# Performance work log

Hardware: AMD Instinct MI355X
Metric: run time of the kernel (lower is better)

## Reference

```python
import jax, jax.numpy as jnp
import numpy as np

N_NODES = 50000
N_EDGES = 50000  # hyperedges
NNZ = 500000
N_GRAPHS = 50
IN_C, HID, OUT_C = 128, 256, 2


def _inv_deg(idx, num_segments):
    deg = jax.ops.segment_sum(jnp.ones(idx.shape[0], jnp.float32), idx, num_segments=num_segments)
    return jnp.where(deg > 0, 1.0 / deg, 0.0)


def hg_conv(x, W, b, rows, cols, dinv, binv):
    # PyG HypergraphConv (no attention, unit edge weights):
    # X' = D^{-1} H B^{-1} H^T (X Theta) + bias
    x = x @ W                                                    # [N, hid]
    e = jax.ops.segment_sum(x[rows], cols, num_segments=N_EDGES) * binv[:, None]   # edge feats [E, hid]
    out = jax.ops.segment_sum(e[cols], rows, num_segments=N_NODES) * dinv[:, None]  # node feats [N, hid]
    return out + b


def setup_inputs() -> dict:
    key = jax.random.key(0)
    ks = jax.random.split(key, 12)
    x = jax.random.normal(ks[0], (N_NODES, IN_C), jnp.float32)
    edge_index = jax.random.randint(ks[1], (2, NNZ), 0, N_EDGES, dtype=jnp.int64)
    batch = jnp.sort(jax.random.randint(ks[2], (N_NODES,), 0, N_GRAPHS, dtype=jnp.int64))
    s = 0.05
    return {
        "x": x, "edge_index": edge_index, "batch": batch,
        "W0": jax.random.normal(ks[3], (IN_C, HID), jnp.float32) * s,
        "b0": jnp.zeros((HID,), jnp.float32),
        "W1": jax.random.normal(ks[4], (HID, HID), jnp.float32) * s,
        "b1": jnp.zeros((HID,), jnp.float32),
        "W2": jax.random.normal(ks[5], (HID, HID), jnp.float32) * s,
        "b2": jnp.zeros((HID,), jnp.float32),
        "M1": jax.random.normal(ks[6], (HID, HID), jnp.float32) * s,
        "bM1": jnp.zeros((HID,), jnp.float32),
        "M2": jax.random.normal(ks[7], (HID, OUT_C), jnp.float32) * s,
        "bM2": jnp.zeros((OUT_C,), jnp.float32),
    }


def reference(x, edge_index, batch, W0, b0, W1, b1, W2, b2, M1, bM1, M2, bM2):
    rows, cols = edge_index[0], edge_index[1]
    dinv = _inv_deg(rows, N_NODES)   # node degree inverse
    binv = _inv_deg(cols, N_EDGES)   # hyperedge degree inverse
    h = jax.nn.relu(hg_conv(x, W0, b0, rows, cols, dinv, binv))
    h = jax.nn.relu(hg_conv(h, W1, b1, rows, cols, dinv, binv))
    h = jax.nn.relu(hg_conv(h, W2, b2, rows, cols, dinv, binv))
    # global_mean_pool (dropout is identity in eval mode)
    cnt = jax.ops.segment_sum(jnp.ones(N_NODES, jnp.float32), batch, num_segments=N_GRAPHS)
    pooled = jax.ops.segment_sum(h, batch, num_segments=N_GRAPHS) / jnp.maximum(cnt, 1.0)[:, None]
    # MLP head
    out = jax.nn.relu(pooled @ M1 + bM1) @ M2 + bM2
    return out
```

## Files before the change

kernel.cpp:

```cpp
#include <hip/hip_runtime.h>
#include <hip/hip_bf16.h>

#define NN   50000
#define NE   50000
#define NNZV 500000
#define NG   50
#define INC  128
#define HID  256
#define OUTC 2
#define STRIDE 32

typedef __bf16 bf16_t;
typedef __bf16 bf16x8 __attribute__((ext_vector_type(8)));
typedef float  f32x4  __attribute__((ext_vector_type(4)));
typedef float  f32x2  __attribute__((ext_vector_type(2)));

__device__ __forceinline__ bf16_t f2b(float f) {
  union { __hip_bfloat16 h; bf16_t b; } u;
  u.h = __float2bfloat16(f);
  return u.b;
}
__device__ __forceinline__ float b2f(bf16_t b) { return (float)b; }

template <bool HI>
__device__ __forceinline__ unsigned int fp8_pk2(float a, float b, unsigned int old) {
  return __builtin_amdgcn_cvt_pk_fp8_f32(a, b, old, HI);
}
__device__ __forceinline__ uint4 fp8_pk16(const float* v) {
  uint4 o;
  unsigned int* ow = &o.x;
#pragma unroll
  for (int wd = 0; wd < 4; wd++) {
    unsigned int u = fp8_pk2<false>(v[wd * 4 + 0], v[wd * 4 + 1], 0u);
    ow[wd] = fp8_pk2<true>(v[wd * 4 + 2], v[wd * 4 + 3], u);
  }
  return o;
}
__device__ __forceinline__ void fp8_acc16(uint4 v, f32x2* a2) {
  a2[0] += __builtin_amdgcn_cvt_pk_f32_fp8(v.x, false);
  a2[1] += __builtin_amdgcn_cvt_pk_f32_fp8(v.x, true);
  a2[2] += __builtin_amdgcn_cvt_pk_f32_fp8(v.y, false);
  a2[3] += __builtin_amdgcn_cvt_pk_f32_fp8(v.y, true);
  a2[4] += __builtin_amdgcn_cvt_pk_f32_fp8(v.z, false);
  a2[5] += __builtin_amdgcn_cvt_pk_f32_fp8(v.z, true);
  a2[6] += __builtin_amdgcn_cvt_pk_f32_fp8(v.w, false);
  a2[7] += __builtin_amdgcn_cvt_pk_f32_fp8(v.w, true);
}

__device__ __forceinline__ void wswiz_one(const float* __restrict__ W, bf16_t* __restrict__ wsw, int t) {
  int lane = t & 63;
  int nt   = (t >> 6) & 15;
  int kc   = t >> 10;
  int q = lane >> 4, n16 = lane & 15;
  bf16x8 o;
#pragma unroll
  for (int j = 0; j < 8; j++)
    o[j] = f2b(W[(size_t)(kc * 32 + q * 8 + j) * HID + nt * 16 + n16]);
  reinterpret_cast<bf16x8*>(wsw)[t] = o;
}

#define FILL_B ((NNZV + 255) / 256)
#define PREP_BX 1563
#define PREP_BW 80
#define PREP_BG 196

__global__ void build_kernel(const int* __restrict__ rows, const int* __restrict__ cols,
                             int* __restrict__ ncur, int* __restrict__ ecur,
                             unsigned short* __restrict__ ncol, unsigned short* __restrict__ erow,
                             const float* __restrict__ x, unsigned char* __restrict__ xb8,
                             const float* __restrict__ W0, const float* __restrict__ W1,
                             const float* __restrict__ W2, bf16_t* __restrict__ w0,
                             bf16_t* __restrict__ w1, bf16_t* __restrict__ w2,
                             const int* __restrict__ batch, int* __restrict__ gstart) {
  int blk = blockIdx.x;
  if (blk < FILL_B) {
    int i = blk * 256 + threadIdx.x;
    if (i < NNZV) {
      int r = rows[i], c = cols[i];
      int pe = atomicAdd(&ecur[c], 1);
      int pn = atomicAdd(&ncur[r], 1);
      if (pe < STRIDE) erow[((size_t)c << 5) + pe] = (unsigned short)r;
      if (pn < STRIDE) ncol[((size_t)r << 5) + pn] = (unsigned short)c;
    }
  } else if (blk < FILL_B + PREP_BX) {
    int t = (blk - FILL_B) * 256 + threadIdx.x;
    if (t >= NN * INC / 16) return;
    const f32x4* p = reinterpret_cast<const f32x4*>(x) + (size_t)t * 4;
    float v[16];
#pragma unroll
    for (int wd = 0; wd < 4; wd++) {
      f32x4 q4 = p[wd];
#pragma unroll
      for (int j = 0; j < 4; j++) v[wd * 4 + j] = q4[j];
    }
    reinterpret_cast<uint4*>(xb8)[t] = fp8_pk16(v);
  } else if (blk < FILL_B + PREP_BX + PREP_BW) {
    int t = (blk - FILL_B - PREP_BX) * 256 + threadIdx.x;
    const int C0 = (INC / 32) * 1024;
    const int C1 = (HID / 32) * 1024;
    if (t < C0)                wswiz_one(W0, w0, t);
    else if (t < C0 + C1)      wswiz_one(W1, w1, t - C0);
    else if (t < C0 + 2 * C1)  wswiz_one(W2, w2, t - C0 - C1);
  } else {
    int i = (blk - FILL_B - PREP_BX - PREP_BW) * 256 + threadIdx.x;
    if (i >= NN) return;
    int cur  = batch[i];
    int prev = (i == 0) ? -1 : batch[i - 1];
    for (int g = prev + 1; g <= cur; g++) gstart[g] = i;
    if (i == NN - 1) {
      for (int g = cur + 1; g <= NG; g++) gstart[g] = NN;
    }
  }
}

template <int K>
__device__ __forceinline__ void gather_direct(const unsigned char* __restrict__ src,
                                              const int* __restrict__ cnt,
                                              const unsigned short* __restrict__ lst,
                                              int seg, int lr, float* acc, int& c) {
  constexpr int LPR = K / 16;
  c = min(cnt[seg], STRIDE);
  const unsigned short* p = lst + ((size_t)seg << 5);
  const uint4* sv = reinterpret_cast<const uint4*>(src);
  f32x2* a2 = reinterpret_cast<f32x2*>(acc);
#pragma unroll
  for (int k = 0; k < 8; k++) a2[k] = f32x2{0.f, 0.f};
  for (int i0 = 0; i0 < c; i0 += 8) {
    int m = c - i0;
    uint4 v[8];
#pragma unroll
    for (int j = 0; j < 8; j++)
      if (j < m) v[j] = sv[(size_t)p[i0 + j] * LPR + lr];
#pragma unroll
    for (int j = 0; j < 8; j++)
      if (j < m) fp8_acc16(v[j], a2);
  }
}

template <int W>
__global__ __launch_bounds__(256) void seg_gather_kernel(const unsigned char* __restrict__ src,
                                                         const int* __restrict__ cnt,
                                                         const unsigned short* __restrict__ lst,
                                                         unsigned char* __restrict__ dst, int nseg) {
  constexpr int LPR = W / 16;
  constexpr int SPW = 64 / LPR;
  constexpr int SPB = 4 * SPW;
  const int lane = threadIdx.x & 63;
  const int wid  = threadIdx.x >> 6;
  const int sub  = lane / LPR, lr = lane % LPR;
  int seg = blockIdx.x * SPB + wid * SPW + sub;
  if (seg >= nseg) return;
  float acc[16];
  int c;
  gather_direct<W>(src, cnt, lst, seg, lr, acc, c);
  float sc = (c > 0) ? (1.0f / (float)c) : 0.f;
  float v16[16];
#pragma unroll
  for (int k = 0; k < 16; k++) v16[k] = acc[k] * sc;
  reinterpret_cast<uint4*>(dst + (size_t)seg * W + lr * 16)[0] = fp8_pk16(v16);
}

template <int K, bool GRELU, bool EPI, bool OUT8>
__global__ __launch_bounds__(256) void ngemm_kernel(const unsigned char* __restrict__ src,
                                                    const int* __restrict__ cnt,
                                                    const unsigned short* __restrict__ lst,
                                                    const float* __restrict__ gbias,
                                                    const bf16_t* __restrict__ wsw,
                                                    const float* __restrict__ ebias,
                                                    void* __restrict__ Bout, int M) {
  constexpr int SW = K + 8;
  __shared__ bf16_t arows[16 * SW];
  const int tid  = threadIdx.x;
  const int wid  = tid >> 6;
  const int lane = tid & 63;
  const int mblk = blockIdx.x * 16;

  constexpr int LPR = K / 16;
  constexpr int SPW = 64 / LPR;
  const int sub = lane / LPR, lr = lane % LPR;
  {
    int row = wid * SPW + sub;
    int seg = mblk + row;
    if (seg < M) {
      float acc[16];
      int c;
      gather_direct<K>(src, cnt, lst, seg, lr, acc, c);
      float sc = (c > 0) ? (1.0f / (float)c) : 0.f;
      bf16_t* dp = arows + row * SW + lr * 16;
      bf16x8 o0, o1;
#pragma unroll
      for (int k = 0; k < 8; k++) {
        float v0 = acc[k] * sc, v1 = acc[k + 8] * sc;
        if constexpr (GRELU) {
          v0 = fmaxf(v0 + gbias[lr * 16 + k], 0.f);
          v1 = fmaxf(v1 + gbias[lr * 16 + k + 8], 0.f);
        }
        o0[k] = f2b(v0);
        o1[k] = f2b(v1);
      }
      reinterpret_cast<bf16x8*>(dp)[0] = o0;
      reinterpret_cast<bf16x8*>(dp)[1] = o1;
    }
  }
  __syncthreads();

  const int q = lane >> 4, n16 = lane & 15;
  f32x4 acc2[4];
#pragma unroll
  for (int j = 0; j < 4; j++) acc2[j] = f32x4{0.f, 0.f, 0.f, 0.f};

  const bf16x8* wv = reinterpret_cast<const bf16x8*>(wsw);
  for (int kc = 0; kc < K / 32; kc++) {
    bf16x8 af = *reinterpret_cast<const bf16x8*>(arows + n16 * SW + kc * 32 + q * 8);
    const bf16x8* wp = wv + (size_t)kc * 1024 + (size_t)(wid * 4) * 64 + lane;
#pragma unroll
    for (int j = 0; j < 4; j++) {
      bf16x8 bf = wp[j * 64];
      acc2[j] = __builtin_amdgcn_mfma_f32_16x16x32_bf16(af, bf, acc2[j], 0, 0, 0);
    }
  }

  float bcol[4];
  if constexpr (EPI) {
#pragma unroll
    for (int j = 0; j < 4; j++) bcol[j] = ebias[(wid * 4 + j) * 16 + n16];
  }

  int mb = mblk + q * 4;
#pragma unroll
  for (int r = 0; r < 4; r++) {
    int m = mb + r;
    if (m < M) {
      if constexpr (OUT8) {
        unsigned char* dst = (unsigned char*)Bout + (size_t)m * HID + n16;
#pragma unroll
        for (int j = 0; j < 4; j++) {
          float v = acc2[j][r];
          if constexpr (EPI) v = fmaxf(v + bcol[j], 0.f);
          unsigned int wbits = fp8_pk2<false>(v, v, 0u);
          dst[(wid * 4 + j) << 4] = (unsigned char)(wbits & 0xffu);
        }
      } else {
        bf16_t* dst = (bf16_t*)Bout + (size_t)m * HID + n16;
#pragma unroll
        for (int j = 0; j < 4; j++) {
          float v = acc2[j][r];
          if constexpr (EPI) v = fmaxf(v + bcol[j], 0.f);
          dst[(wid * 4 + j) << 4] = f2b(v);
        }
      }
    }
  }
}

template <int K>
__global__ __launch_bounds__(256) void ngemm2_kernel(const unsigned char* __restrict__ src,
                                                     const int* __restrict__ cnt,
                                                     const unsigned short* __restrict__ lst,
                                                     const bf16_t* __restrict__ wswA,
                                                     const float* __restrict__ biasA,
                                                     const bf16_t* __restrict__ wswB,
                                                     unsigned char* __restrict__ Bout, int M) {
  constexpr int SW  = K + 8;
  constexpr int SW2 = HID + 8;
  constexpr int LPR = K / 16;
  constexpr int SPW = 64 / LPR;
  __shared__ bf16_t arows[32 * SW];
  __shared__ bf16_t brows[32 * SW2];
  const int tid  = threadIdx.x;
  const int wid  = tid >> 6;
  const int lane = tid & 63;
  const int mblk = blockIdx.x * 32;

  {
    const int sub = lane / LPR, lr = lane % LPR;
    int row = wid * SPW + sub;
    int seg = mblk + row;
    if (seg < M) {
      float acc[16];
      int c;
      gather_direct<K>(src, cnt, lst, seg, lr, acc, c);
      float sc = (c > 0) ? (1.0f / (float)c) : 0.f;
      bf16_t* dp = arows + row * SW + lr * 16;
      bf16x8 o0, o1;
#pragma unroll
      for (int k = 0; k < 8; k++) {
        o0[k] = f2b(acc[k] * sc);
        o1[k] = f2b(acc[k + 8] * sc);
      }
      reinterpret_cast<bf16x8*>(dp)[0] = o0;
      reinterpret_cast<bf16x8*>(dp)[1] = o1;
    }
  }
  __syncthreads();

  const int q = lane >> 4, n16 = lane & 15;
  {
    f32x4 acc2[2][4];
#pragma unroll
    for (int a = 0; a < 2; a++)
#pragma unroll
      for (int j = 0; j < 4; j++) acc2[a][j] = f32x4{0.f, 0.f, 0.f, 0.f};
    const bf16x8* wv = reinterpret_cast<const bf16x8*>(wswA);
    for (int kc = 0; kc < K / 32; kc++) {
      bf16x8 af0 = *reinterpret_cast<const bf16x8*>(arows + n16 * SW + kc * 32 + q * 8);
      bf16x8 af1 = *reinterpret_cast<const bf16x8*>(arows + (n16 + 16) * SW + kc * 32 + q * 8);
      const bf16x8* wp = wv + (size_t)kc * 1024 + (size_t)(wid * 4) * 64 + lane;
#pragma unroll
      for (int j = 0; j < 4; j++) {
        bf16x8 bf = wp[j * 64];
        acc2[0][j] = __builtin_amdgcn_mfma_f32_16x16x32_bf16(af0, bf, acc2[0][j], 0, 0, 0);
        acc2[1][j] = __builtin_amdgcn_mfma_f32_16x16x32_bf16(af1, bf, acc2[1][j], 0, 0, 0);
      }
    }
#pragma unroll
    for (int a = 0; a < 2; a++) {
#pragma unroll
      for (int j = 0; j < 4; j++) {
        float bj = biasA[(wid * 4 + j) * 16 + n16];
#pragma unroll
        for (int r = 0; r < 4; r++) {
          float v = fmaxf(acc2[a][j][r] + bj, 0.f);
          brows[(a * 16 + q * 4 + r) * SW2 + (wid * 4 + j) * 16 + n16] = f2b(v);
        }
      }
    }
  }
  __syncthreads();

  f32x4 acc3[2][4];
#pragma unroll
  for (int a = 0; a < 2; a++)
#pragma unroll
    for (int j = 0; j < 4; j++) acc3[a][j] = f32x4{0.f, 0.f, 0.f, 0.f};
  const bf16x8* wv = reinterpret_cast<const bf16x8*>(wswB);
  for (int kc = 0; kc < HID / 32; kc++) {
    bf16x8 af0 = *reinterpret_cast<const bf16x8*>(brows + n16 * SW2 + kc * 32 + q * 8);
    bf16x8 af1 = *reinterpret_cast<const bf16x8*>(brows + (n16 + 16) * SW2 + kc * 32 + q * 8);
    const bf16x8* wp = wv + (size_t)kc * 1024 + (size_t)(wid * 4) * 64 + lane;
#pragma unroll
    for (int j = 0; j < 4; j++) {
      bf16x8 bf = wp[j * 64];
      acc3[0][j] = __builtin_amdgcn_mfma_f32_16x16x32_bf16(af0, bf, acc3[0][j], 0, 0, 0);
      acc3[1][j] = __builtin_amdgcn_mfma_f32_16x16x32_bf16(af1, bf, acc3[1][j], 0, 0, 0);
    }
  }

#pragma unroll
  for (int a = 0; a < 2; a++) {
    int mb = mblk + a * 16 + q * 4;
#pragma unroll
    for (int r = 0; r < 4; r++) {
      int m = mb + r;
      if (m < M) {
        unsigned char* dst = Bout + (size_t)m * HID + n16;
#pragma unroll
        for (int j = 0; j < 4; j++) {
          float v = acc3[a][j][r];
          unsigned int wbits = fp8_pk2<false>(v, v, 0u);
          dst[(wid * 4 + j) << 4] = (unsigned char)(wbits & 0xffu);
        }
      }
    }
  }
}

__global__ __launch_bounds__(256) void npool_kernel(const unsigned char* __restrict__ src,
                                                    const int* __restrict__ cnt,
                                                    const unsigned short* __restrict__ lst,
                                                    const float* __restrict__ bias,
                                                    const int* __restrict__ batch,
                                                    float* __restrict__ pooled) {
  constexpr int K = HID, SW = K + 8;
  __shared__ bf16_t arows[16 * SW];
  const int tid  = threadIdx.x;
  const int wid  = tid >> 6;
  const int lane = tid & 63;
  const int mblk = blockIdx.x * 16;

  constexpr int LPR = K / 16;
  constexpr int SPW = 64 / LPR;
  const int sub = lane / LPR, lr = lane % LPR;
  {
    int row = wid * SPW + sub;
    int seg = mblk + row;
    if (seg < NN) {
      float acc[16];
      int c;
      gather_direct<K>(src, cnt, lst, seg, lr, acc, c);
      float sc = (c > 0) ? (1.0f / (float)c) : 0.f;
      bf16_t* dp = arows + row * SW + lr * 16;
      bf16x8 o0, o1;
#pragma unroll
      for (int k = 0; k < 8; k++) {
        o0[k] = f2b(fmaxf(acc[k] * sc + bias[lr * 16 + k], 0.f));
        o1[k] = f2b(fmaxf(acc[k + 8] * sc + bias[lr * 16 + k + 8], 0.f));
      }
      reinterpret_cast<bf16x8*>(dp)[0] = o0;
      reinterpret_cast<bf16x8*>(dp)[1] = o1;
    }
  }
  __syncthreads();

  int f = tid;
  float acc = 0.f;
  int curg = -1;
  for (int r = 0; r < 16; r++) {
    int node = mblk + r;
    if (node >= NN) break;
    int g = batch[node];
    if (g != curg) {
      if (curg >= 0) atomicAdd(&pooled[(size_t)curg * HID + f], acc);
      curg = g; acc = 0.f;
    }
    acc += b2f(arows[r * SW + f]);
  }
  if (curg >= 0) atomicAdd(&pooled[(size_t)curg * HID + f], acc);
}

__global__ void head_kernel(const float* __restrict__ pooled, const int* __restrict__ gstart,
                            const float* __restrict__ M1, const float* __restrict__ bM1,
                            const float* __restrict__ M2, const float* __restrict__ bM2,
                            float* __restrict__ out) {
  int g = blockIdx.x;
  int t = threadIdx.x;
  __shared__ float p[HID];
  __shared__ float red[256];
  float cntf = (float)(gstart[g + 1] - gstart[g]);
  float inv = 1.f / fmaxf(cntf, 1.f);
  p[t] = pooled[(size_t)g * HID + t] * inv;
  __syncthreads();
  float h = bM1[t];
  for (int k = 0; k < HID; k++) h += p[k] * M1[k * HID + t];
  h = fmaxf(h, 0.f);
  float c0 = h * M2[t * OUTC + 0];
  float c1 = h * M2[t * OUTC + 1];
  red[t] = c0;
  __syncthreads();
  for (int off = 128; off > 0; off >>= 1) {
    if (t < off) red[t] += red[t + off];
    __syncthreads();
  }
  float s0 = 0.f;
  if (t == 0) s0 = red[0];
  __syncthreads();
  red[t] = c1;
  __syncthreads();
  for (int off = 128; off > 0; off >>= 1) {
    if (t < off) red[t] += red[t + off];
    __syncthreads();
  }
  if (t == 0) {
    out[g * 2 + 0] = s0 + bM2[0];
    out[g * 2 + 1] = red[0] + bM2[1];
  }
}

extern "C" void kernel_launch(void* const* d_in, const int* in_sizes, int n_in,
                              void* d_out, int out_size, void* d_ws, size_t ws_size,
                              hipStream_t stream) {
  const float* x   = (const float*)d_in[0];
  const int* ei    = (const int*)d_in[1];
  const int* rows  = ei;
  const int* cols  = ei + NNZV;
  const int* batch = (const int*)d_in[2];
  const float* W0  = (const float*)d_in[3];
  const float* b0  = (const float*)d_in[4];
  const float* W1  = (const float*)d_in[5];
  const float* b1  = (const float*)d_in[6];
  const float* W2  = (const float*)d_in[7];
  const float* b2  = (const float*)d_in[8];
  const float* M1  = (const float*)d_in[9];
  const float* bM1 = (const float*)d_in[10];
  const float* M2  = (const float*)d_in[11];
  const float* bM2 = (const float*)d_in[12];
  float* out       = (float*)d_out;

  char* w = (char*)d_ws;
  size_t off = 0;
  bf16_t* P = (bf16_t*)(w + off); off += (size_t)NN * HID * 2;
  bf16_t* Q = (bf16_t*)(w + off); off += (size_t)NE * HID * 2;
  bf16_t* R = (bf16_t*)(w + off); off += (size_t)NN * HID * 2;
  bf16_t* wsw0 = (bf16_t*)(w + off); off += (size_t)INC * HID * 2;
  bf16_t* wsw1 = (bf16_t*)(w + off); off += (size_t)HID * HID * 2;
  bf16_t* wsw2 = (bf16_t*)(w + off); off += (size_t)HID * HID * 2;
  int* gstart   = (int*)(w + off);   off += (size_t)(NG + 1) * 4;
  size_t zoff = off;
  float* pooled = (float*)(w + off); off += (size_t)NG * HID * 4;
  int* ncur     = (int*)(w + off);   off += (size_t)NN * 4;
  int* ecur     = (int*)(w + off);   off += (size_t)NE * 4;
  size_t zbytes = off - zoff;
  off = (off + 63) & ~(size_t)63;
  unsigned short* erow = (unsigned short*)(w + off); off += (size_t)NE * STRIDE * 2;
  unsigned short* ncol = (unsigned short*)(w + off); off += (size_t)NN * STRIDE * 2;

  unsigned char* xb8 = (unsigned char*)R;
  unsigned char* Qe8 = (unsigned char*)Q;
  unsigned char* Q8  = (unsigned char*)Q;
  unsigned char* P8  = (unsigned char*)P;

  (void)hipMemsetAsync(w + zoff, 0, zbytes, stream);

  const int BN = 256;
  build_kernel<<<FILL_B + PREP_BX + PREP_BW + PREP_BG, BN, 0, stream>>>(
      rows, cols, ncur, ecur, ncol, erow, x, xb8, W0, W1, W2, wsw0, wsw1, wsw2, batch, gstart);

  seg_gather_kernel<INC><<<(NE + 31) / 32, BN, 0, stream>>>(xb8, ecur, erow, Qe8, NE);
  ngemm2_kernel<INC><<<(NN + 31) / 32, BN, 0, stream>>>(Qe8, ncur, ncol, wsw0, b0, wsw1, P8, NN);
  seg_gather_kernel<HID><<<(NE + 15) / 16, BN, 0, stream>>>(P8, ecur, erow, Q8, NE);
  ngemm_kernel<HID, true, false, true><<<(NN + 15) / 16, BN, 0, stream>>>(
      Q8, ncur, ncol, b1, wsw2, nullptr, P8, NN);
  seg_gather_kernel<HID><<<(NE + 15) / 16, BN, 0, stream>>>(P8, ecur, erow, Q8, NE);
  npool_kernel<<<(NN + 15) / 16, BN, 0, stream>>>(Q8, ncur, ncol, b2, batch, pooled);

  head_kernel<<<NG, 256, 0, stream>>>(pooled, gstart, M1, bM1, M2, bM2, out);
}
```

Before: 364.2 us.

## Partition CSR fill atomics by XCD using index low bits

Splits the adjacency-list build into separate edge-list and node-list passes, each replicated over 8 block groups that only handle indices whose low 3 bits match the block's position mod 8. This aims to keep atomic counter updates and list writes for a given index local to one XCD's L2 on a multi-die GPU, reducing cross-die atomic traffic. In exchange, every block rereads the rows/cols input 16 times and many more blocks are launched, with most threads doing no atomic work.

After: 332.5 us. -8.7%, faster.

```diff
diff --git a/kernel.cpp b/kernel.cpp
--- a/kernel.cpp
+++ b/kernel.cpp
@@ -59,7 +59,10 @@
   reinterpret_cast<bf16x8*>(wsw)[t] = o;
 }
 
-#define FILL_B ((NNZV + 255) / 256)
+#define FILL_EPT   2
+#define FILL_CHUNK (256 * FILL_EPT)
+#define FILL_NCH   ((NNZV + FILL_CHUNK - 1) / FILL_CHUNK)
+#define FILL_B     (FILL_NCH * 8)
 #define PREP_BX 1563
 #define PREP_BW 80
 #define PREP_BG 196
@@ -73,17 +76,32 @@
                              bf16_t* __restrict__ w1, bf16_t* __restrict__ w2,
                              const int* __restrict__ batch, int* __restrict__ gstart) {
   int blk = blockIdx.x;
-  if (blk < FILL_B) {
-    int i = blk * 256 + threadIdx.x;
-    if (i < NNZV) {
-      int r = rows[i], c = cols[i];
-      int pe = atomicAdd(&ecur[c], 1);
-      int pn = atomicAdd(&ncur[r], 1);
-      if (pe < STRIDE) erow[((size_t)c << 5) + pe] = (unsigned short)r;
-      if (pn < STRIDE) ncol[((size_t)r << 5) + pn] = (unsigned short)c;
-    }
-  } else if (blk < FILL_B + PREP_BX) {
-    int t = (blk - FILL_B) * 256 + threadIdx.x;
+  if (blk < 2 * FILL_B) {
+    bool ner = blk >= FILL_B;
+    int local = ner ? blk - FILL_B : blk;
+    int vx    = local & 7;
+    int chunk = local >> 3;
+    int base  = chunk * FILL_CHUNK + threadIdx.x;
+#pragma unroll
+    for (int e = 0; e < FILL_EPT; e++) {
+      int i = base + e * 256;
+      if (i < NNZV) {
+        int r = rows[i], c = cols[i];
+        if (!ner) {
+          if ((c & 7) == vx) {
+            int pe = atomicAdd(&ecur[c], 1);
+            if (pe < STRIDE) erow[((size_t)c << 5) + pe] = (unsigned short)r;
+          }
+        } else {
+          if ((r & 7) == vx) {
+            int pn = atomicAdd(&ncur[r], 1);
+            if (pn < STRIDE) ncol[((size_t)r << 5) + pn] = (unsigned short)c;
+          }
+        }
+      }
+    }
+  } else if (blk < 2 * FILL_B + PREP_BX) {
+    int t = (blk - 2 * FILL_B) * 256 + threadIdx.x;
     if (t >= NN * INC / 16) return;
     const f32x4* p = reinterpret_cast<const f32x4*>(x) + (size_t)t * 4;
     float v[16];
@@ -94,15 +112,15 @@
       for (int j = 0; j < 4; j++) v[wd * 4 + j] = q4[j];
     }
     reinterpret_cast<uint4*>(xb8)[t] = fp8_pk16(v);
-  } else if (blk < FILL_B + PREP_BX + PREP_BW) {
-    int t = (blk - FILL_B - PREP_BX) * 256 + threadIdx.x;
+  } else if (blk < 2 * FILL_B + PREP_BX + PREP_BW) {
+    int t = (blk - 2 * FILL_B - PREP_BX) * 256 + threadIdx.x;
     const int C0 = (INC / 32) * 1024;
     const int C1 = (HID / 32) * 1024;
     if (t < C0)                wswiz_one(W0, w0, t);
     else if (t < C0 + C1)      wswiz_one(W1, w1, t - C0);
     else if (t < C0 + 2 * C1)  wswiz_one(W2, w2, t - C0 - C1);
   } else {
-    int i = (blk - FILL_B - PREP_BX - PREP_BW) * 256 + threadIdx.x;
+    int i = (blk - 2 * FILL_B - PREP_BX - PREP_BW) * 256 + threadIdx.x;
     if (i >= NN) return;
     int cur  = batch[i];
     int prev = (i == 0) ? -1 : batch[i - 1];
@@ -502,7 +520,7 @@
   (void)hipMemsetAsync(w + zoff, 0, zbytes, stream);
 
   const int BN = 256;
-  build_kernel<<<FILL_B + PREP_BX + PREP_BW + PREP_BG, BN, 0, stream>>>(
+  build_kernel<<<2 * FILL_B + PREP_BX + PREP_BW + PREP_BG, BN, 0, stream>>>(
       rows, cols, ncur, ecur, ncol, erow, x, xb8, W0, W1, W2, wsw0, wsw1, wsw2, batch, gstart);
 
   seg_gather_kernel<INC><<<(NE + 31) / 32, BN, 0, stream>>>(xb8, ecur, erow, Qe8, NE);
```
